# Kernel tuning notes

Hardware: AMD Instinct MI355X
Metric: run time of the kernel (lower is better)

## Reference

```python
import jax, jax.numpy as jnp
import numpy as np

NUM_GRAPHS = 256
N_NODES = 128          # nodes per graph (equal-size graphs)
DEG = 16               # average degree
NUM_EDGES = NUM_GRAPHS * N_NODES * DEG
NUM_HEADS = 8
SCALE = 10.0
INF_REPLACE = 1.0


def setup_inputs() -> dict:
    key = jax.random.key(0)
    k1, k2, k3 = jax.random.split(key, 3)
    # each graph owns a contiguous block of N_NODES global node ids
    eg = jnp.repeat(jnp.arange(NUM_GRAPHS, dtype=jnp.int32), N_NODES * DEG)
    src_loc = jax.random.randint(k1, (NUM_EDGES,), 0, N_NODES, dtype=jnp.int32)
    dst_loc = jax.random.randint(k2, (NUM_EDGES,), 0, N_NODES, dtype=jnp.int32)
    edge_index = jnp.stack([eg * N_NODES + src_loc, eg * N_NODES + dst_loc])  # [2, E]
    edge_weight = jax.random.uniform(k3, (NUM_EDGES,), minval=0.1, maxval=1.0)
    batch = jnp.repeat(jnp.arange(NUM_GRAPHS, dtype=jnp.int32), N_NODES)  # [N_total]
    return {
        'edge_index': edge_index,
        'edge_weight': edge_weight,
        'batch': batch,
        'num_graphs': NUM_GRAPHS,
        'max_num_nodes': N_NODES,
    }


def _shortest_path_bias(edge_index, edge_weight, batch, num_graphs, max_num_nodes):
    G, n = num_graphs, max_num_nodes
    inf = jnp.inf
    # per-graph node offsets (graphs occupy contiguous node-id blocks)
    counts = jnp.bincount(batch, length=G)
    offsets = jnp.concatenate([jnp.zeros((1,), counts.dtype), jnp.cumsum(counts)[:-1]])
    src, dst = edge_index[0], edge_index[1]
    eg = batch[src]                              # graph id of each edge
    u = src - offsets[eg]                        # local node ids
    v = dst - offsets[eg]
    # self-loops are skipped in the original (masked to +inf -> no-op under min)
    w = jnp.where(src == dst, inf, edge_weight)

    # init dense distance: inf off-diagonal, 0 on diagonal, edge weights scattered
    dist = jnp.full((G, n, n), inf, dtype=edge_weight.dtype)
    diag = jnp.arange(n)
    dist = dist.at[:, diag, diag].set(0.0)
    dist = dist.at[eg, u, v].min(w)

    # batched Floyd-Warshall: d[i,j] = min(d[i,j], d[i,k] + d[k,j]) for all graphs
    def body(d, k):
        col = jax.lax.dynamic_slice_in_dim(d, k, 1, axis=2)  # [G, n, 1] = d[:, :, k]
        row = jax.lax.dynamic_slice_in_dim(d, k, 1, axis=1)  # [G, 1, n] = d[:, k, :]
        return jnp.minimum(d, col + row), None
    dist, _ = jax.lax.scan(body, dist, jnp.arange(n))

    # replace unreachable with 2 * max finite distance (per graph)
    finite = jnp.isfinite(dist)
    fmax = jnp.max(jnp.where(finite, dist, -inf), axis=(1, 2), keepdims=True)
    unreach = jnp.where(jnp.isfinite(fmax), 2.0 * fmax, INF_REPLACE)
    dist = jnp.where(finite, dist, unreach)

    # normalize per graph and scale
    max_val = jnp.maximum(jnp.max(dist, axis=(1, 2), keepdims=True), 1e-8)
    bias = -SCALE * (dist / max_val)
    bias = jnp.nan_to_num(bias, nan=0.0, posinf=-1e6, neginf=-1e6)

    # expand over heads and flatten to [B*H, n, n]
    bias = jnp.broadcast_to(bias[:, None], (G, NUM_HEADS, n, n))
    return bias.reshape(G * NUM_HEADS, n, n)


def reference(edge_index, edge_weight, batch, num_graphs, max_num_nodes):
    return _shortest_path_bias(edge_index, edge_weight, batch, num_graphs, max_num_nodes)
```

## Files before the change

### kernel.cpp

```cpp
#include <hip/hip_runtime.h>

#define NHEADS 8
#define NN     128
#define NCELL  (NN * NN)
#define NT     512
#define SCALE_F 10.0f

typedef float nfloat4 __attribute__((ext_vector_type(4)));

#define RP_O 0
#define RP_N 2048
#define CP_As 4096
#define CP_Bs 6208
#define DP   8320
#define RED  8640

template<int CBN>
__device__ __forceinline__ void extract_panels(const float (&dd)[4][8], float* lds,
                                               const int kbn, const int t,
                                               const int rgrp, const int cgrp,
                                               const int cpbase)
{
    if ((rgrp >> 2) == kbn) {
        const int q = rgrp & 3;
        #pragma unroll
        for (int rr = 0; rr < 4; ++rr) {
            const int iloc = 4 * q + rr;
            #pragma unroll
            for (int c = 0; c < 2; ++c) {
                *reinterpret_cast<float4*>(
                    &lds[RP_O + iloc * 128 + (cgrp << 2) + (c << 6)]) =
                    make_float4(dd[rr][c*4+0], dd[rr][c*4+1],
                                dd[rr][c*4+2], dd[rr][c*4+3]);
            }
        }
        const int p = cgrp - 4 * (kbn & 3);
        if ((unsigned)p < 4u) {
            #pragma unroll
            for (int rr = 0; rr < 4; ++rr) {
                *reinterpret_cast<float4*>(&lds[DP + (4*q+rr) * 20 + (p << 2)]) =
                    make_float4(dd[rr][CBN+0], dd[rr][CBN+1],
                                dd[rr][CBN+2], dd[rr][CBN+3]);
            }
        }
    }
    {
        const int q2 = cgrp - 4 * (kbn & 3);
        if ((unsigned)q2 < 4u) {
            #pragma unroll
            for (int e = 0; e < 4; ++e) {
                const int m = 4 * q2 + e;
                *reinterpret_cast<float4*>(&lds[cpbase + m * 132 + (rgrp << 2)]) =
                    make_float4(dd[0][CBN+e], dd[1][CBN+e],
                                dd[2][CBN+e], dd[3][CBN+e]);
            }
        }
    }
}

__device__ __forceinline__ void closure(float* lds, const int t, const int kb)
{
    if ((t >> 6) == kb) {
        asm volatile("s_waitcnt lgkmcnt(0)" ::: "memory");
        const int l  = t & 63;
        const int i  = l & 15;
        const int jq = l >> 4;
        float4 v = *reinterpret_cast<const float4*>(&lds[DP + i*20 + (jq << 2)]);
        float T0 = v.x, T1 = v.y, T2 = v.z, T3 = v.w;
        #pragma unroll
        for (int k = 0; k < 16; ++k) {
            const int ksrc = ((k >> 2) << 4) | i;
            float dik;
            switch (k & 3) {
                case 0: dik = __shfl(T0, ksrc); break;
                case 1: dik = __shfl(T1, ksrc); break;
                case 2: dik = __shfl(T2, ksrc); break;
                default: dik = __shfl(T3, ksrc); break;
            }
            const int rsrc = (jq << 4) | k;
            const float r0 = __shfl(T0, rsrc);
            const float r1 = __shfl(T1, rsrc);
            const float r2 = __shfl(T2, rsrc);
            const float r3 = __shfl(T3, rsrc);
            T0 = fminf(T0, dik + r0);
            T1 = fminf(T1, dik + r1);
            T2 = fminf(T2, dik + r2);
            T3 = fminf(T3, dik + r3);
        }
        *reinterpret_cast<float4*>(&lds[DP + i*20 + (jq << 2)]) =
            make_float4(T0, T1, T2, T3);
    }
}

__device__ __forceinline__ void bprime(float* lds, const int t)
{
    if (t < 256) {
        const float INF = __builtin_huge_valf();
        const int k2 = t >> 5;
        const int ch = t & 31;
        float4 R[16];
        #pragma unroll
        for (int m = 0; m < 16; ++m)
            R[m] = *reinterpret_cast<const float4*>(&lds[RP_O + m*128 + (ch<<2)]);
        float da[16], db[16];
        #pragma unroll
        for (int c4 = 0; c4 < 4; ++c4) {
            float4 va = *reinterpret_cast<const float4*>(&lds[DP + (2*k2  )*20 + (c4<<2)]);
            float4 vb = *reinterpret_cast<const float4*>(&lds[DP + (2*k2+1)*20 + (c4<<2)]);
            da[c4*4+0]=va.x; da[c4*4+1]=va.y; da[c4*4+2]=va.z; da[c4*4+3]=va.w;
            db[c4*4+0]=vb.x; db[c4*4+1]=vb.y; db[c4*4+2]=vb.z; db[c4*4+3]=vb.w;
        }
        float aA[4] = {INF, INF, INF, INF};
        float aB[4] = {INF, INF, INF, INF};
        #pragma unroll
        for (int mp = 0; mp < 8; ++mp) {
            const int m0 = 2*mp, m1 = 2*mp + 1;
            const float rv0[4] = {R[m0].x, R[m0].y, R[m0].z, R[m0].w};
            const float rv1[4] = {R[m1].x, R[m1].y, R[m1].z, R[m1].w};
            #pragma unroll
            for (int e = 0; e < 4; ++e) {
                aA[e] = fminf(fminf(aA[e], da[m0] + rv0[e]), da[m1] + rv1[e]);
                aB[e] = fminf(fminf(aB[e], db[m0] + rv0[e]), db[m1] + rv1[e]);
            }
        }
        *reinterpret_cast<float4*>(&lds[RP_N + (2*k2  )*128 + (ch<<2)]) =
            make_float4(aA[0], aA[1], aA[2], aA[3]);
        *reinterpret_cast<float4*>(&lds[RP_N + (2*k2+1)*128 + (ch<<2)]) =
            make_float4(aB[0], aB[1], aB[2], aB[3]);
    }
}

__device__ __forceinline__ void cphase(float (&dd)[4][8], float* lds,
                                       const int rgrp, const int cgrp,
                                       const int cpbase)
{
    #pragma unroll
    for (int mq = 0; mq < 4; ++mq) {
        float4 cp[4], ra[4], rb[4];
        #pragma unroll
        for (int e = 0; e < 4; ++e) {
            const int m = 4*mq + e;
            cp[e] = *reinterpret_cast<const float4*>(&lds[cpbase + m*132 + (rgrp<<2)]);
            ra[e] = *reinterpret_cast<const float4*>(&lds[RP_N + m*128 + (cgrp<<2)]);
            rb[e] = *reinterpret_cast<const float4*>(&lds[RP_N + m*128 + (cgrp<<2) + 64]);
        }
        #pragma unroll
        for (int e2 = 0; e2 < 2; ++e2) {
            const float c0[4]  = {cp[2*e2].x, cp[2*e2].y, cp[2*e2].z, cp[2*e2].w};
            const float c1[4]  = {cp[2*e2+1].x, cp[2*e2+1].y, cp[2*e2+1].z, cp[2*e2+1].w};
            const float ra0[4] = {ra[2*e2].x, ra[2*e2].y, ra[2*e2].z, ra[2*e2].w};
            const float ra1[4] = {ra[2*e2+1].x, ra[2*e2+1].y, ra[2*e2+1].z, ra[2*e2+1].w};
            const float rb0[4] = {rb[2*e2].x, rb[2*e2].y, rb[2*e2].z, rb[2*e2].w};
            const float rb1[4] = {rb[2*e2+1].x, rb[2*e2+1].y, rb[2*e2+1].z, rb[2*e2+1].w};
            #pragma unroll
            for (int rr = 0; rr < 4; ++rr) {
                #pragma unroll
                for (int e = 0; e < 4; ++e) {
                    dd[rr][e]   = fminf(fminf(dd[rr][e],   c0[rr] + ra0[e]), c1[rr] + ra1[e]);
                    dd[rr][4+e] = fminf(fminf(dd[rr][4+e], c0[rr] + rb0[e]), c1[rr] + rb1[e]);
                }
            }
        }
    }
}

__global__ __launch_bounds__(NT, 2)
void spb_fw_kernel(const int* __restrict__ edge_index,
                   const float* __restrict__ edge_weight,
                   const int num_edges, const int epg,
                   float* __restrict__ out)
{
    __shared__ float lds[NCELL];
    const float INF = __builtin_huge_valf();
    const int t    = threadIdx.x;
    const int g    = blockIdx.x;
    const int cgrp = t & 15;
    const int rgrp = t >> 4;

    const int ebase = g * epg;
    int esrc[4], edst[4]; float ew[4];
    #pragma unroll
    for (int k = 0; k < 4; ++k) {
        int e = t + k * NT;
        e = (e < epg) ? e : (epg - 1);
        const int idx = ebase + e;
        esrc[k] = edge_index[idx];
        edst[k] = edge_index[num_edges + idx];
        ew[k]   = edge_weight[idx];
    }

    #pragma unroll
    for (int c = 0; c < 8; ++c) {
        const int m   = t + (c << 9);
        const int i   = m >> 5;
        const int scm = m & 31;
        const int c0  = (scm ^ (i & 7)) << 2;
        float4 v;
        v.x = (c0 + 0 == i) ? 0.0f : INF;
        v.y = (c0 + 1 == i) ? 0.0f : INF;
        v.z = (c0 + 2 == i) ? 0.0f : INF;
        v.w = (c0 + 3 == i) ? 0.0f : INF;
        *reinterpret_cast<float4*>(&lds[m << 2]) = v;
    }
    __syncthreads();

    #pragma unroll
    for (int k = 0; k < 4; ++k) {
        const int u = esrc[k] - g * NN;
        const int v = edst[k] - g * NN;
        if (u != v && (unsigned)u < (unsigned)NN && (unsigned)v < (unsigned)NN) {
            const int a = (u << 7) + (v ^ ((u & 7) << 2));
            atomicMin(reinterpret_cast<int*>(&lds[a]), __float_as_int(ew[k]));
        }
    }
    __syncthreads();

    float dd[4][8];
    #pragma unroll
    for (int rr = 0; rr < 4; ++rr) {
        const int i = (rgrp << 2) + rr;
        const int s = i & 7;
        #pragma unroll
        for (int c = 0; c < 2; ++c) {
            float4 v = *reinterpret_cast<const float4*>(
                &lds[(i << 7) + (((cgrp + 16*c) ^ s) << 2)]);
            dd[rr][c*4+0]=v.x; dd[rr][c*4+1]=v.y; dd[rr][c*4+2]=v.z; dd[rr][c*4+3]=v.w;
        }
    }
    __syncthreads();

    extract_panels<0>(dd, lds, 0, t, rgrp, cgrp, CP_As);
    #pragma unroll 1
    for (int kb = 0; kb < 8; ++kb) {
        closure(lds, t, kb);
        __syncthreads();
        bprime(lds, t);
        __syncthreads();
        cphase(dd, lds, rgrp, cgrp, (kb & 1) ? CP_Bs : CP_As);
        if (kb < 7) {
            const int kbn = kb + 1;
            const int cpb = (kbn & 1) ? CP_Bs : CP_As;
            if (kbn < 4) extract_panels<0>(dd, lds, kbn, t, rgrp, cgrp, cpb);
            else         extract_panels<4>(dd, lds, kbn, t, rgrp, cgrp, cpb);
        }
    }
    __syncthreads();

    float mF = 0.0f, mA = 0.0f;
    #pragma unroll
    for (int rr = 0; rr < 4; ++rr)
        #pragma unroll
        for (int j = 0; j < 8; ++j) {
            const float v = dd[rr][j];
            mA = fmaxf(mA, v);
            mF = fmaxf(mF, v < INF ? v : 0.0f);
        }
    #pragma unroll
    for (int o = 32; o > 0; o >>= 1) {
        mF = fmaxf(mF, __shfl_xor(mF, o));
        mA = fmaxf(mA, __shfl_xor(mA, o));
    }
    if ((t & 63) == 0) {
        lds[RED + ((t >> 6) << 1)]     = mF;
        lds[RED + ((t >> 6) << 1) + 1] = mA;
    }
    __syncthreads();
    mF = lds[RED]; mA = lds[RED + 1];
    #pragma unroll
    for (int wv = 1; wv < 8; ++wv) {
        mF = fmaxf(mF, lds[RED + wv*2]);
        mA = fmaxf(mA, lds[RED + wv*2 + 1]);
    }
    const float twoF  = 2.0f * mF;
    const float maxv  = fmaxf((mA == INF) ? twoF : mF, 1e-8f);
    const float nscal = -SCALE_F / maxv;

    float* const outg = out + (size_t)g * (NHEADS * NCELL);
    #pragma unroll
    for (int rr = 0; rr < 4; ++rr) {
        const int i = (rgrp << 2) + rr;
        #pragma unroll
        for (int c = 0; c < 2; ++c) {
            nfloat4 v;
            v.x = ((dd[rr][c*4+0] == INF) ? twoF : dd[rr][c*4+0]) * nscal;
            v.y = ((dd[rr][c*4+1] == INF) ? twoF : dd[rr][c*4+1]) * nscal;
            v.z = ((dd[rr][c*4+2] == INF) ? twoF : dd[rr][c*4+2]) * nscal;
            v.w = ((dd[rr][c*4+3] == INF) ? twoF : dd[rr][c*4+3]) * nscal;
            const int o = (i << 7) + (cgrp << 2) + (c << 6);
            #pragma unroll
            for (int h = 0; h < NHEADS; ++h) {
                __builtin_nontemporal_store(
                    v, reinterpret_cast<nfloat4*>(&outg[h * NCELL + o]));
            }
        }
    }
}

extern "C" void kernel_launch(void* const* d_in, const int* in_sizes, int n_in,
                              void* d_out, int out_size, void* d_ws, size_t ws_size,
                              hipStream_t stream)
{
    const int*   edge_index  = (const int*)d_in[0];
    const float* edge_w      = (const float*)d_in[1];
    const int E    = in_sizes[1];
    const int Ntot = in_sizes[2];
    const int G    = Ntot / NN;
    const int epg  = E / G;
    float* out = (float*)d_out;
    spb_fw_kernel<<<G, NT, 0, stream>>>(edge_index, edge_w, E, epg, out);
}
```

Measured before the change: 61.65 us.

## Double threads per block and fuse closure with B-panel update

Doubles the block to 1024 threads so each thread holds a 4x4 tile of the distance matrix instead of 4x8, which halves the per-thread C-phase work and register footprint. The diagonal closure and the row-panel (bprime) update are merged into one function run by the first four waves, with each wave redoing the closure redundantly, so one barrier per block step is removed. A barrier is added after panel extraction instead. The risk is that the 1024-thread block and the extra redundant closure work could limit occupancy or add idle waves during the serial phases.

```diff
diff --git a/kernel.cpp b/kernel.cpp
--- a/kernel.cpp
+++ b/kernel.cpp
@@ -3,7 +3,7 @@
 #define NHEADS 8
 #define NN     128
 #define NCELL  (NN * NN)
-#define NT     512
+#define NT     1024
 #define SCALE_F 10.0f
 
 typedef float nfloat4 __attribute__((ext_vector_type(4)));
@@ -12,60 +12,48 @@
 #define RP_N 2048
 #define CP_As 4096
 #define CP_Bs 6208
-#define DP   8320
+#define DPS  8320
 #define RED  8640
 
-template<int CBN>
-__device__ __forceinline__ void extract_panels(const float (&dd)[4][8], float* lds,
-                                               const int kbn, const int t,
-                                               const int rgrp, const int cgrp,
-                                               const int cpbase)
+__device__ __forceinline__ void extract_panels(const float (&dd)[4][4], float* lds,
+                                               const int kbn, const int rgrp,
+                                               const int cgrp, const int cpbase)
 {
     if ((rgrp >> 2) == kbn) {
-        const int q = rgrp & 3;
+        const int qb = (rgrp & 3) << 2;
         #pragma unroll
         for (int rr = 0; rr < 4; ++rr) {
-            const int iloc = 4 * q + rr;
-            #pragma unroll
-            for (int c = 0; c < 2; ++c) {
-                *reinterpret_cast<float4*>(
-                    &lds[RP_O + iloc * 128 + (cgrp << 2) + (c << 6)]) =
-                    make_float4(dd[rr][c*4+0], dd[rr][c*4+1],
-                                dd[rr][c*4+2], dd[rr][c*4+3]);
-            }
-        }
-        const int p = cgrp - 4 * (kbn & 3);
-        if ((unsigned)p < 4u) {
+            *reinterpret_cast<float4*>(&lds[RP_O + (qb+rr)*128 + (cgrp<<2)]) =
+                make_float4(dd[rr][0], dd[rr][1], dd[rr][2], dd[rr][3]);
+        }
+        if ((cgrp >> 2) == kbn) {
+            const int p = (cgrp & 3) << 2;
             #pragma unroll
             for (int rr = 0; rr < 4; ++rr) {
-                *reinterpret_cast<float4*>(&lds[DP + (4*q+rr) * 20 + (p << 2)]) =
-                    make_float4(dd[rr][CBN+0], dd[rr][CBN+1],
-                                dd[rr][CBN+2], dd[rr][CBN+3]);
-            }
-        }
-    }
-    {
-        const int q2 = cgrp - 4 * (kbn & 3);
-        if ((unsigned)q2 < 4u) {
-            #pragma unroll
-            for (int e = 0; e < 4; ++e) {
-                const int m = 4 * q2 + e;
-                *reinterpret_cast<float4*>(&lds[cpbase + m * 132 + (rgrp << 2)]) =
-                    make_float4(dd[0][CBN+e], dd[1][CBN+e],
-                                dd[2][CBN+e], dd[3][CBN+e]);
-            }
-        }
-    }
-}
-
-__device__ __forceinline__ void closure(float* lds, const int t, const int kb)
-{
-    if ((t >> 6) == kb) {
-        asm volatile("s_waitcnt lgkmcnt(0)" ::: "memory");
+                *reinterpret_cast<float4*>(&lds[DPS + (qb+rr)*20 + p]) =
+                    make_float4(dd[rr][0], dd[rr][1], dd[rr][2], dd[rr][3]);
+            }
+        }
+    }
+    if ((cgrp >> 2) == kbn) {
+        const int mb = (cgrp & 3) << 2;
+        #pragma unroll
+        for (int e = 0; e < 4; ++e) {
+            *reinterpret_cast<float4*>(&lds[cpbase + (mb+e)*132 + (rgrp<<2)]) =
+                make_float4(dd[0][e], dd[1][e], dd[2][e], dd[3][e]);
+        }
+    }
+}
+
+__device__ __forceinline__ void closure_bprime(float* lds, const int t)
+{
+    if (t < 256) {
+        const float INF = __builtin_huge_valf();
         const int l  = t & 63;
         const int i  = l & 15;
         const int jq = l >> 4;
-        float4 v = *reinterpret_cast<const float4*>(&lds[DP + i*20 + (jq << 2)]);
+        const int w  = t >> 6;
+        float4 v = *reinterpret_cast<const float4*>(&lds[DPS + i*20 + (jq<<2)]);
         float T0 = v.x, T1 = v.y, T2 = v.z, T3 = v.w;
         #pragma unroll
         for (int k = 0; k < 16; ++k) {
@@ -87,84 +75,75 @@
             T2 = fminf(T2, dik + r2);
             T3 = fminf(T3, dik + r3);
         }
-        *reinterpret_cast<float4*>(&lds[DP + i*20 + (jq << 2)]) =
+        *reinterpret_cast<float4*>(&lds[DPS + i*20 + (jq<<2)]) =
             make_float4(T0, T1, T2, T3);
-    }
-}
-
-__device__ __forceinline__ void bprime(float* lds, const int t)
-{
-    if (t < 256) {
-        const float INF = __builtin_huge_valf();
-        const int k2 = t >> 5;
-        const int ch = t & 31;
-        float4 R[16];
-        #pragma unroll
-        for (int m = 0; m < 16; ++m)
-            R[m] = *reinterpret_cast<const float4*>(&lds[RP_O + m*128 + (ch<<2)]);
-        float da[16], db[16];
-        #pragma unroll
-        for (int c4 = 0; c4 < 4; ++c4) {
-            float4 va = *reinterpret_cast<const float4*>(&lds[DP + (2*k2  )*20 + (c4<<2)]);
-            float4 vb = *reinterpret_cast<const float4*>(&lds[DP + (2*k2+1)*20 + (c4<<2)]);
-            da[c4*4+0]=va.x; da[c4*4+1]=va.y; da[c4*4+2]=va.z; da[c4*4+3]=va.w;
-            db[c4*4+0]=vb.x; db[c4*4+1]=vb.y; db[c4*4+2]=vb.z; db[c4*4+3]=vb.w;
-        }
-        float aA[4] = {INF, INF, INF, INF};
-        float aB[4] = {INF, INF, INF, INF};
+        asm volatile("s_waitcnt lgkmcnt(0)" ::: "memory");
+        const int r  = (w << 2) | jq;
+        const int j0 = i << 3;
+        float da[16];
+        #pragma unroll
+        for (int q = 0; q < 4; ++q) {
+            float4 d4 = *reinterpret_cast<const float4*>(&lds[DPS + r*20 + (q<<2)]);
+            da[4*q+0]=d4.x; da[4*q+1]=d4.y; da[4*q+2]=d4.z; da[4*q+3]=d4.w;
+        }
+        float aA[8];
+        #pragma unroll
+        for (int e = 0; e < 8; ++e) aA[e] = INF;
         #pragma unroll
         for (int mp = 0; mp < 8; ++mp) {
             const int m0 = 2*mp, m1 = 2*mp + 1;
-            const float rv0[4] = {R[m0].x, R[m0].y, R[m0].z, R[m0].w};
-            const float rv1[4] = {R[m1].x, R[m1].y, R[m1].z, R[m1].w};
+            float4 ra0 = *reinterpret_cast<const float4*>(&lds[RP_O + m0*128 + j0]);
+            float4 ra1 = *reinterpret_cast<const float4*>(&lds[RP_O + m0*128 + j0 + 4]);
+            float4 rb0 = *reinterpret_cast<const float4*>(&lds[RP_O + m1*128 + j0]);
+            float4 rb1 = *reinterpret_cast<const float4*>(&lds[RP_O + m1*128 + j0 + 4]);
+            const float a0[4] = {ra0.x, ra0.y, ra0.z, ra0.w};
+            const float a1[4] = {ra1.x, ra1.y, ra1.z, ra1.w};
+            const float b0[4] = {rb0.x, rb0.y, rb0.z, rb0.w};
+            const float b1[4] = {rb1.x, rb1.y, rb1.z, rb1.w};
             #pragma unroll
             for (int e = 0; e < 4; ++e) {
-                aA[e] = fminf(fminf(aA[e], da[m0] + rv0[e]), da[m1] + rv1[e]);
-                aB[e] = fminf(fminf(aB[e], db[m0] + rv0[e]), db[m1] + rv1[e]);
-            }
-        }
-        *reinterpret_cast<float4*>(&lds[RP_N + (2*k2  )*128 + (ch<<2)]) =
+                aA[e]   = fminf(fminf(aA[e],   da[m0] + a0[e]), da[m1] + b0[e]);
+                aA[4+e] = fminf(fminf(aA[4+e], da[m0] + a1[e]), da[m1] + b1[e]);
+            }
+        }
+        *reinterpret_cast<float4*>(&lds[RP_N + r*128 + j0]) =
             make_float4(aA[0], aA[1], aA[2], aA[3]);
-        *reinterpret_cast<float4*>(&lds[RP_N + (2*k2+1)*128 + (ch<<2)]) =
-            make_float4(aB[0], aB[1], aB[2], aB[3]);
-    }
-}
-
-__device__ __forceinline__ void cphase(float (&dd)[4][8], float* lds,
+        *reinterpret_cast<float4*>(&lds[RP_N + r*128 + j0 + 4]) =
+            make_float4(aA[4], aA[5], aA[6], aA[7]);
+    }
+}
+
+__device__ __forceinline__ void cphase(float (&dd)[4][4], float* lds,
                                        const int rgrp, const int cgrp,
                                        const int cpbase)
 {
     #pragma unroll
     for (int mq = 0; mq < 4; ++mq) {
-        float4 cp[4], ra[4], rb[4];
+        float4 cp[4], ra[4];
         #pragma unroll
         for (int e = 0; e < 4; ++e) {
             const int m = 4*mq + e;
             cp[e] = *reinterpret_cast<const float4*>(&lds[cpbase + m*132 + (rgrp<<2)]);
             ra[e] = *reinterpret_cast<const float4*>(&lds[RP_N + m*128 + (cgrp<<2)]);
-            rb[e] = *reinterpret_cast<const float4*>(&lds[RP_N + m*128 + (cgrp<<2) + 64]);
-        }
-        #pragma unroll
-        for (int e2 = 0; e2 < 2; ++e2) {
-            const float c0[4]  = {cp[2*e2].x, cp[2*e2].y, cp[2*e2].z, cp[2*e2].w};
-            const float c1[4]  = {cp[2*e2+1].x, cp[2*e2+1].y, cp[2*e2+1].z, cp[2*e2+1].w};
-            const float ra0[4] = {ra[2*e2].x, ra[2*e2].y, ra[2*e2].z, ra[2*e2].w};
-            const float ra1[4] = {ra[2*e2+1].x, ra[2*e2+1].y, ra[2*e2+1].z, ra[2*e2+1].w};
-            const float rb0[4] = {rb[2*e2].x, rb[2*e2].y, rb[2*e2].z, rb[2*e2].w};
-            const float rb1[4] = {rb[2*e2+1].x, rb[2*e2+1].y, rb[2*e2+1].z, rb[2*e2+1].w};
+        }
+        #pragma unroll
+        for (int ee = 0; ee < 2; ++ee) {
+            const float c0[4] = {cp[2*ee].x, cp[2*ee].y, cp[2*ee].z, cp[2*ee].w};
+            const float c1[4] = {cp[2*ee+1].x, cp[2*ee+1].y, cp[2*ee+1].z, cp[2*ee+1].w};
+            const float r0[4] = {ra[2*ee].x, ra[2*ee].y, ra[2*ee].z, ra[2*ee].w};
+            const float r1[4] = {ra[2*ee+1].x, ra[2*ee+1].y, ra[2*ee+1].z, ra[2*ee+1].w};
             #pragma unroll
             for (int rr = 0; rr < 4; ++rr) {
                 #pragma unroll
                 for (int e = 0; e < 4; ++e) {
-                    dd[rr][e]   = fminf(fminf(dd[rr][e],   c0[rr] + ra0[e]), c1[rr] + ra1[e]);
-                    dd[rr][4+e] = fminf(fminf(dd[rr][4+e], c0[rr] + rb0[e]), c1[rr] + rb1[e]);
+                    dd[rr][e] = fminf(fminf(dd[rr][e], c0[rr] + r0[e]), c1[rr] + r1[e]);
                 }
             }
         }
     }
 }
 
-__global__ __launch_bounds__(NT, 2)
+__global__ __launch_bounds__(NT, 4)
 void spb_fw_kernel(const int* __restrict__ edge_index,
                    const float* __restrict__ edge_weight,
                    const int num_edges, const int epg,
@@ -174,24 +153,23 @@
     const float INF = __builtin_huge_valf();
     const int t    = threadIdx.x;
     const int g    = blockIdx.x;
-    const int cgrp = t & 15;
-    const int rgrp = t >> 4;
+    const int cgrp = t & 31;
+    const int rgrp = t >> 5;
 
     const int ebase = g * epg;
-    int esrc[4], edst[4]; float ew[4];
-    #pragma unroll
-    for (int k = 0; k < 4; ++k) {
-        int e = t + k * NT;
+    int es[2], ed[2]; float ewt[2];
+    #pragma unroll
+    for (int k = 0; k < 2; ++k) {
+        int e = t + (k << 10);
         e = (e < epg) ? e : (epg - 1);
-        const int idx = ebase + e;
-        esrc[k] = edge_index[idx];
-        edst[k] = edge_index[num_edges + idx];
-        ew[k]   = edge_weight[idx];
-    }
-
-    #pragma unroll
-    for (int c = 0; c < 8; ++c) {
-        const int m   = t + (c << 9);
+        es[k]  = edge_index[ebase + e];
+        ed[k]  = edge_index[num_edges + ebase + e];
+        ewt[k] = edge_weight[ebase + e];
+    }
+
+    #pragma unroll
+    for (int c = 0; c < 4; ++c) {
+        const int m   = t + (c << 10);
         const int i   = m >> 5;
         const int scm = m & 31;
         const int c0  = (scm ^ (i & 7)) << 2;
@@ -205,52 +183,43 @@
     __syncthreads();
 
     #pragma unroll
-    for (int k = 0; k < 4; ++k) {
-        const int u = esrc[k] - g * NN;
-        const int v = edst[k] - g * NN;
+    for (int k = 0; k < 2; ++k) {
+        const int u = es[k] - g * NN;
+        const int v = ed[k] - g * NN;
         if (u != v && (unsigned)u < (unsigned)NN && (unsigned)v < (unsigned)NN) {
             const int a = (u << 7) + (v ^ ((u & 7) << 2));
-            atomicMin(reinterpret_cast<int*>(&lds[a]), __float_as_int(ew[k]));
-        }
-    }
-    __syncthreads();
-
-    float dd[4][8];
+            atomicMin(reinterpret_cast<int*>(&lds[a]), __float_as_int(ewt[k]));
+        }
+    }
+    __syncthreads();
+
+    float dd[4][4];
     #pragma unroll
     for (int rr = 0; rr < 4; ++rr) {
         const int i = (rgrp << 2) + rr;
-        const int s = i & 7;
-        #pragma unroll
-        for (int c = 0; c < 2; ++c) {
-            float4 v = *reinterpret_cast<const float4*>(
-                &lds[(i << 7) + (((cgrp + 16*c) ^ s) << 2)]);
-            dd[rr][c*4+0]=v.x; dd[rr][c*4+1]=v.y; dd[rr][c*4+2]=v.z; dd[rr][c*4+3]=v.w;
-        }
-    }
-    __syncthreads();
-
-    extract_panels<0>(dd, lds, 0, t, rgrp, cgrp, CP_As);
+        float4 v = *reinterpret_cast<const float4*>(
+            &lds[(i << 7) + ((cgrp ^ (i & 7)) << 2)]);
+        dd[rr][0]=v.x; dd[rr][1]=v.y; dd[rr][2]=v.z; dd[rr][3]=v.w;
+    }
+    __syncthreads();
+
+    extract_panels(dd, lds, 0, rgrp, cgrp, CP_As);
+    __syncthreads();
     #pragma unroll 1
     for (int kb = 0; kb < 8; ++kb) {
-        closure(lds, t, kb);
-        __syncthreads();
-        bprime(lds, t);
+        closure_bprime(lds, t);
         __syncthreads();
         cphase(dd, lds, rgrp, cgrp, (kb & 1) ? CP_Bs : CP_As);
-        if (kb < 7) {
-            const int kbn = kb + 1;
-            const int cpb = (kbn & 1) ? CP_Bs : CP_As;
-            if (kbn < 4) extract_panels<0>(dd, lds, kbn, t, rgrp, cgrp, cpb);
-            else         extract_panels<4>(dd, lds, kbn, t, rgrp, cgrp, cpb);
-        }
-    }
-    __syncthreads();
+        if (kb < 7)
+            extract_panels(dd, lds, kb + 1, rgrp, cgrp, ((kb+1) & 1) ? CP_Bs : CP_As);
+        __syncthreads();
+    }
 
     float mF = 0.0f, mA = 0.0f;
     #pragma unroll
     for (int rr = 0; rr < 4; ++rr)
         #pragma unroll
-        for (int j = 0; j < 8; ++j) {
+        for (int j = 0; j < 4; ++j) {
             const float v = dd[rr][j];
             mA = fmaxf(mA, v);
             mF = fmaxf(mF, v < INF ? v : 0.0f);
@@ -267,7 +236,7 @@
     __syncthreads();
     mF = lds[RED]; mA = lds[RED + 1];
     #pragma unroll
-    for (int wv = 1; wv < 8; ++wv) {
+    for (int wv = 1; wv < 16; ++wv) {
         mF = fmaxf(mF, lds[RED + wv*2]);
         mA = fmaxf(mA, lds[RED + wv*2 + 1]);
     }
@@ -279,19 +248,16 @@
     #pragma unroll
     for (int rr = 0; rr < 4; ++rr) {
         const int i = (rgrp << 2) + rr;
-        #pragma unroll
-        for (int c = 0; c < 2; ++c) {
-            nfloat4 v;
-            v.x = ((dd[rr][c*4+0] == INF) ? twoF : dd[rr][c*4+0]) * nscal;
-            v.y = ((dd[rr][c*4+1] == INF) ? twoF : dd[rr][c*4+1]) * nscal;
-            v.z = ((dd[rr][c*4+2] == INF) ? twoF : dd[rr][c*4+2]) * nscal;
-            v.w = ((dd[rr][c*4+3] == INF) ? twoF : dd[rr][c*4+3]) * nscal;
-            const int o = (i << 7) + (cgrp << 2) + (c << 6);
-            #pragma unroll
-            for (int h = 0; h < NHEADS; ++h) {
-                __builtin_nontemporal_store(
-                    v, reinterpret_cast<nfloat4*>(&outg[h * NCELL + o]));
-            }
+        nfloat4 v;
+        v.x = ((dd[rr][0] == INF) ? twoF : dd[rr][0]) * nscal;
+        v.y = ((dd[rr][1] == INF) ? twoF : dd[rr][1]) * nscal;
+        v.z = ((dd[rr][2] == INF) ? twoF : dd[rr][2]) * nscal;
+        v.w = ((dd[rr][3] == INF) ? twoF : dd[rr][3]) * nscal;
+        const int o = (i << 7) + (cgrp << 2);
+        #pragma unroll
+        for (int h = 0; h < NHEADS; ++h) {
+            __builtin_nontemporal_store(
+                v, reinterpret_cast<nfloat4*>(&outg[h * NCELL + o]));
         }
     }
 }
```

After: 67.46 us. 1.09x slower.

## Run blocked Floyd-Warshall in packed fp16 with contiguous 8-column thread tiles

Applied to the files above, without the earlier changes.

Stores the per-thread distance tile and the row and column panels as packed half-precision vectors and does the min-plus updates with packed fp16 add/min. Each thread now owns 8 contiguous columns instead of two split groups of 4, and LDS panel layouts are resized to match. The aim is to halve LDS traffic and double ALU throughput in the b-prime and c-phase updates. Distances lose precision with fp16 rounding and range, which may break tolerance against the fp32 reference.

```diff
diff --git a/kernel.cpp b/kernel.cpp
--- a/kernel.cpp
+++ b/kernel.cpp
@@ -6,54 +6,47 @@
 #define NT     512
 #define SCALE_F 10.0f
 
-typedef float nfloat4 __attribute__((ext_vector_type(4)));
-
-#define RP_O 0
-#define RP_N 2048
-#define CP_As 4096
-#define CP_Bs 6208
-#define DP   8320
-#define RED  8640
-
-template<int CBN>
-__device__ __forceinline__ void extract_panels(const float (&dd)[4][8], float* lds,
-                                               const int kbn, const int t,
+typedef float    nfloat4 __attribute__((ext_vector_type(4)));
+typedef _Float16 h4      __attribute__((ext_vector_type(4)));
+typedef _Float16 h8      __attribute__((ext_vector_type(8)));
+
+#define RPAD   136
+#define RP_O_H 0
+#define RP_N_H 2176
+#define CP_A_H 4352
+#define CP_B_H 6464
+#define DPS_F  4400
+#define RED_F  4720
+
+__device__ __forceinline__ void extract_panels(const h8 (&dd)[4], float* lds,
+                                               _Float16* ldsH, const int kbn,
                                                const int rgrp, const int cgrp,
-                                               const int cpbase)
+                                               const int cpH)
 {
     if ((rgrp >> 2) == kbn) {
-        const int q = rgrp & 3;
-        #pragma unroll
-        for (int rr = 0; rr < 4; ++rr) {
-            const int iloc = 4 * q + rr;
-            #pragma unroll
-            for (int c = 0; c < 2; ++c) {
-                *reinterpret_cast<float4*>(
-                    &lds[RP_O + iloc * 128 + (cgrp << 2) + (c << 6)]) =
-                    make_float4(dd[rr][c*4+0], dd[rr][c*4+1],
-                                dd[rr][c*4+2], dd[rr][c*4+3]);
-            }
-        }
-        const int p = cgrp - 4 * (kbn & 3);
-        if ((unsigned)p < 4u) {
+        const int qb = (rgrp & 3) << 2;
+        #pragma unroll
+        for (int rr = 0; rr < 4; ++rr)
+            *reinterpret_cast<h8*>(ldsH + RP_O_H + (qb+rr)*RPAD + (cgrp << 3)) = dd[rr];
+        if ((cgrp >> 1) == kbn) {
+            const int p = (cgrp & 1) << 3;
             #pragma unroll
             for (int rr = 0; rr < 4; ++rr) {
-                *reinterpret_cast<float4*>(&lds[DP + (4*q+rr) * 20 + (p << 2)]) =
-                    make_float4(dd[rr][CBN+0], dd[rr][CBN+1],
-                                dd[rr][CBN+2], dd[rr][CBN+3]);
+                *reinterpret_cast<float4*>(&lds[DPS_F + (qb+rr)*20 + p]) =
+                    make_float4((float)dd[rr][0], (float)dd[rr][1],
+                                (float)dd[rr][2], (float)dd[rr][3]);
+                *reinterpret_cast<float4*>(&lds[DPS_F + (qb+rr)*20 + p + 4]) =
+                    make_float4((float)dd[rr][4], (float)dd[rr][5],
+                                (float)dd[rr][6], (float)dd[rr][7]);
             }
         }
     }
-    {
-        const int q2 = cgrp - 4 * (kbn & 3);
-        if ((unsigned)q2 < 4u) {
-            #pragma unroll
-            for (int e = 0; e < 4; ++e) {
-                const int m = 4 * q2 + e;
-                *reinterpret_cast<float4*>(&lds[cpbase + m * 132 + (rgrp << 2)]) =
-                    make_float4(dd[0][CBN+e], dd[1][CBN+e],
-                                dd[2][CBN+e], dd[3][CBN+e]);
-            }
+    if ((cgrp >> 1) == kbn) {
+        const int lcb = (cgrp & 1) << 3;
+        #pragma unroll
+        for (int e = 0; e < 8; ++e) {
+            h4 v = {dd[0][e], dd[1][e], dd[2][e], dd[3][e]};
+            *reinterpret_cast<h4*>(ldsH + cpH + (lcb+e)*132 + (rgrp << 2)) = v;
         }
     }
 }
@@ -65,7 +58,7 @@
         const int l  = t & 63;
         const int i  = l & 15;
         const int jq = l >> 4;
-        float4 v = *reinterpret_cast<const float4*>(&lds[DP + i*20 + (jq << 2)]);
+        float4 v = *reinterpret_cast<const float4*>(&lds[DPS_F + i*20 + (jq << 2)]);
         float T0 = v.x, T1 = v.y, T2 = v.z, T3 = v.w;
         #pragma unroll
         for (int k = 0; k < 16; ++k) {
@@ -87,80 +80,44 @@
             T2 = fminf(T2, dik + r2);
             T3 = fminf(T3, dik + r3);
         }
-        *reinterpret_cast<float4*>(&lds[DP + i*20 + (jq << 2)]) =
+        *reinterpret_cast<float4*>(&lds[DPS_F + i*20 + (jq << 2)]) =
             make_float4(T0, T1, T2, T3);
     }
 }
 
-__device__ __forceinline__ void bprime(float* lds, const int t)
+__device__ __forceinline__ void bprime(float* lds, _Float16* ldsH, const int t)
 {
     if (t < 256) {
-        const float INF = __builtin_huge_valf();
-        const int k2 = t >> 5;
-        const int ch = t & 31;
-        float4 R[16];
-        #pragma unroll
-        for (int m = 0; m < 16; ++m)
-            R[m] = *reinterpret_cast<const float4*>(&lds[RP_O + m*128 + (ch<<2)]);
-        float da[16], db[16];
-        #pragma unroll
-        for (int c4 = 0; c4 < 4; ++c4) {
-            float4 va = *reinterpret_cast<const float4*>(&lds[DP + (2*k2  )*20 + (c4<<2)]);
-            float4 vb = *reinterpret_cast<const float4*>(&lds[DP + (2*k2+1)*20 + (c4<<2)]);
-            da[c4*4+0]=va.x; da[c4*4+1]=va.y; da[c4*4+2]=va.z; da[c4*4+3]=va.w;
-            db[c4*4+0]=vb.x; db[c4*4+1]=vb.y; db[c4*4+2]=vb.z; db[c4*4+3]=vb.w;
-        }
-        float aA[4] = {INF, INF, INF, INF};
-        float aB[4] = {INF, INF, INF, INF};
-        #pragma unroll
-        for (int mp = 0; mp < 8; ++mp) {
-            const int m0 = 2*mp, m1 = 2*mp + 1;
-            const float rv0[4] = {R[m0].x, R[m0].y, R[m0].z, R[m0].w};
-            const float rv1[4] = {R[m1].x, R[m1].y, R[m1].z, R[m1].w};
-            #pragma unroll
-            for (int e = 0; e < 4; ++e) {
-                aA[e] = fminf(fminf(aA[e], da[m0] + rv0[e]), da[m1] + rv1[e]);
-                aB[e] = fminf(fminf(aB[e], db[m0] + rv0[e]), db[m1] + rv1[e]);
-            }
-        }
-        *reinterpret_cast<float4*>(&lds[RP_N + (2*k2  )*128 + (ch<<2)]) =
-            make_float4(aA[0], aA[1], aA[2], aA[3]);
-        *reinterpret_cast<float4*>(&lds[RP_N + (2*k2+1)*128 + (ch<<2)]) =
-            make_float4(aB[0], aB[1], aB[2], aB[3]);
-    }
-}
-
-__device__ __forceinline__ void cphase(float (&dd)[4][8], float* lds,
-                                       const int rgrp, const int cgrp,
-                                       const int cpbase)
-{
-    #pragma unroll
-    for (int mq = 0; mq < 4; ++mq) {
-        float4 cp[4], ra[4], rb[4];
-        #pragma unroll
-        for (int e = 0; e < 4; ++e) {
-            const int m = 4*mq + e;
-            cp[e] = *reinterpret_cast<const float4*>(&lds[cpbase + m*132 + (rgrp<<2)]);
-            ra[e] = *reinterpret_cast<const float4*>(&lds[RP_N + m*128 + (cgrp<<2)]);
-            rb[e] = *reinterpret_cast<const float4*>(&lds[RP_N + m*128 + (cgrp<<2) + 64]);
-        }
-        #pragma unroll
-        for (int e2 = 0; e2 < 2; ++e2) {
-            const float c0[4]  = {cp[2*e2].x, cp[2*e2].y, cp[2*e2].z, cp[2*e2].w};
-            const float c1[4]  = {cp[2*e2+1].x, cp[2*e2+1].y, cp[2*e2+1].z, cp[2*e2+1].w};
-            const float ra0[4] = {ra[2*e2].x, ra[2*e2].y, ra[2*e2].z, ra[2*e2].w};
-            const float ra1[4] = {ra[2*e2+1].x, ra[2*e2+1].y, ra[2*e2+1].z, ra[2*e2+1].w};
-            const float rb0[4] = {rb[2*e2].x, rb[2*e2].y, rb[2*e2].z, rb[2*e2].w};
-            const float rb1[4] = {rb[2*e2+1].x, rb[2*e2+1].y, rb[2*e2+1].z, rb[2*e2+1].w};
-            #pragma unroll
-            for (int rr = 0; rr < 4; ++rr) {
-                #pragma unroll
-                for (int e = 0; e < 4; ++e) {
-                    dd[rr][e]   = fminf(fminf(dd[rr][e],   c0[rr] + ra0[e]), c1[rr] + ra1[e]);
-                    dd[rr][4+e] = fminf(fminf(dd[rr][4+e], c0[rr] + rb0[e]), c1[rr] + rb1[e]);
-                }
-            }
-        }
+        const int r  = t >> 4;
+        const int j8 = t & 15;
+        float da[16];
+        #pragma unroll
+        for (int q = 0; q < 4; ++q) {
+            float4 d4 = *reinterpret_cast<const float4*>(&lds[DPS_F + r*20 + (q << 2)]);
+            da[4*q+0]=d4.x; da[4*q+1]=d4.y; da[4*q+2]=d4.z; da[4*q+3]=d4.w;
+        }
+        h8 acc = (h8)(_Float16)__builtin_huge_valf();
+        #pragma unroll
+        for (int m = 0; m < 16; ++m) {
+            h8 rv = *reinterpret_cast<const h8*>(ldsH + RP_O_H + m*RPAD + (j8 << 3));
+            h8 d2 = (h8)(_Float16)da[m];
+            acc = __builtin_elementwise_min(acc, d2 + rv);
+        }
+        *reinterpret_cast<h8*>(ldsH + RP_N_H + r*RPAD + (j8 << 3)) = acc;
+    }
+}
+
+__device__ __forceinline__ void cphase(h8 (&dd)[4], _Float16* ldsH,
+                                       const int rgrp, const int cgrp, const int cpH)
+{
+    #pragma unroll
+    for (int m = 0; m < 16; ++m) {
+        h4 c4 = *reinterpret_cast<const h4*>(ldsH + cpH + m*132 + (rgrp << 2));
+        h8 r8 = *reinterpret_cast<const h8*>(ldsH + RP_N_H + m*RPAD + (cgrp << 3));
+        dd[0] = __builtin_elementwise_min(dd[0], (h8)(c4[0]) + r8);
+        dd[1] = __builtin_elementwise_min(dd[1], (h8)(c4[1]) + r8);
+        dd[2] = __builtin_elementwise_min(dd[2], (h8)(c4[2]) + r8);
+        dd[3] = __builtin_elementwise_min(dd[3], (h8)(c4[3]) + r8);
     }
 }
 
@@ -171,6 +128,7 @@
                    float* __restrict__ out)
 {
     __shared__ float lds[NCELL];
+    _Float16* const ldsH = reinterpret_cast<_Float16*>(lds);
     const float INF = __builtin_huge_valf();
     const int t    = threadIdx.x;
     const int g    = blockIdx.x;
@@ -215,34 +173,32 @@
     }
     __syncthreads();
 
-    float dd[4][8];
+    h8 dd[4];
     #pragma unroll
     for (int rr = 0; rr < 4; ++rr) {
         const int i = (rgrp << 2) + rr;
         const int s = i & 7;
-        #pragma unroll
-        for (int c = 0; c < 2; ++c) {
-            float4 v = *reinterpret_cast<const float4*>(
-                &lds[(i << 7) + (((cgrp + 16*c) ^ s) << 2)]);
-            dd[rr][c*4+0]=v.x; dd[rr][c*4+1]=v.y; dd[rr][c*4+2]=v.z; dd[rr][c*4+3]=v.w;
-        }
-    }
-    __syncthreads();
-
-    extract_panels<0>(dd, lds, 0, t, rgrp, cgrp, CP_As);
+        const int q0 = cgrp << 1;
+        float4 a = *reinterpret_cast<const float4*>(&lds[(i << 7) + (((q0  ) ^ s) << 2)]);
+        float4 b = *reinterpret_cast<const float4*>(&lds[(i << 7) + (((q0+1) ^ s) << 2)]);
+        h8 v;
+        v[0]=(_Float16)a.x; v[1]=(_Float16)a.y; v[2]=(_Float16)a.z; v[3]=(_Float16)a.w;
+        v[4]=(_Float16)b.x; v[5]=(_Float16)b.y; v[6]=(_Float16)b.z; v[7]=(_Float16)b.w;
+        dd[rr] = v;
+    }
+    __syncthreads();
+
+    extract_panels(dd, lds, ldsH, 0, rgrp, cgrp, CP_A_H);
     #pragma unroll 1
     for (int kb = 0; kb < 8; ++kb) {
         closure(lds, t, kb);
         __syncthreads();
-        bprime(lds, t);
+        bprime(lds, ldsH, t);
         __syncthreads();
-        cphase(dd, lds, rgrp, cgrp, (kb & 1) ? CP_Bs : CP_As);
-        if (kb < 7) {
-            const int kbn = kb + 1;
-            const int cpb = (kbn & 1) ? CP_Bs : CP_As;
-            if (kbn < 4) extract_panels<0>(dd, lds, kbn, t, rgrp, cgrp, cpb);
-            else         extract_panels<4>(dd, lds, kbn, t, rgrp, cgrp, cpb);
-        }
+        cphase(dd, ldsH, rgrp, cgrp, (kb & 1) ? CP_B_H : CP_A_H);
+        if (kb < 7)
+            extract_panels(dd, lds, ldsH, kb + 1, rgrp, cgrp,
+                           ((kb + 1) & 1) ? CP_B_H : CP_A_H);
     }
     __syncthreads();
 
@@ -250,10 +206,10 @@
     #pragma unroll
     for (int rr = 0; rr < 4; ++rr)
         #pragma unroll
-        for (int j = 0; j < 8; ++j) {
-            const float v = dd[rr][j];
-            mA = fmaxf(mA, v);
-            mF = fmaxf(mF, v < INF ? v : 0.0f);
+        for (int e = 0; e < 8; ++e) {
+            const float f = (float)dd[rr][e];
+            mA = fmaxf(mA, f);
+            mF = fmaxf(mF, f < INF ? f : 0.0f);
         }
     #pragma unroll
     for (int o = 32; o > 0; o >>= 1) {
@@ -261,15 +217,15 @@
         mA = fmaxf(mA, __shfl_xor(mA, o));
     }
     if ((t & 63) == 0) {
-        lds[RED + ((t >> 6) << 1)]     = mF;
-        lds[RED + ((t >> 6) << 1) + 1] = mA;
-    }
-    __syncthreads();
-    mF = lds[RED]; mA = lds[RED + 1];
+        lds[RED_F + ((t >> 6) << 1)]     = mF;
+        lds[RED_F + ((t >> 6) << 1) + 1] = mA;
+    }
+    __syncthreads();
+    mF = lds[RED_F]; mA = lds[RED_F + 1];
     #pragma unroll
     for (int wv = 1; wv < 8; ++wv) {
-        mF = fmaxf(mF, lds[RED + wv*2]);
-        mA = fmaxf(mA, lds[RED + wv*2 + 1]);
+        mF = fmaxf(mF, lds[RED_F + wv*2]);
+        mA = fmaxf(mA, lds[RED_F + wv*2 + 1]);
     }
     const float twoF  = 2.0f * mF;
     const float maxv  = fmaxf((mA == INF) ? twoF : mF, 1e-8f);
@@ -279,19 +235,20 @@
     #pragma unroll
     for (int rr = 0; rr < 4; ++rr) {
         const int i = (rgrp << 2) + rr;
-        #pragma unroll
-        for (int c = 0; c < 2; ++c) {
-            nfloat4 v;
-            v.x = ((dd[rr][c*4+0] == INF) ? twoF : dd[rr][c*4+0]) * nscal;
-            v.y = ((dd[rr][c*4+1] == INF) ? twoF : dd[rr][c*4+1]) * nscal;
-            v.z = ((dd[rr][c*4+2] == INF) ? twoF : dd[rr][c*4+2]) * nscal;
-            v.w = ((dd[rr][c*4+3] == INF) ? twoF : dd[rr][c*4+3]) * nscal;
-            const int o = (i << 7) + (cgrp << 2) + (c << 6);
-            #pragma unroll
-            for (int h = 0; h < NHEADS; ++h) {
-                __builtin_nontemporal_store(
-                    v, reinterpret_cast<nfloat4*>(&outg[h * NCELL + o]));
-            }
+        float f[8];
+        #pragma unroll
+        for (int e = 0; e < 8; ++e) {
+            const float x = (float)dd[rr][e];
+            f[e] = ((x == INF) ? twoF : x) * nscal;
+        }
+        nfloat4 va, vb;
+        va.x=f[0]; va.y=f[1]; va.z=f[2]; va.w=f[3];
+        vb.x=f[4]; vb.y=f[5]; vb.z=f[6]; vb.w=f[7];
+        const int o = (i << 7) + (cgrp << 3);
+        #pragma unroll
+        for (int h = 0; h < NHEADS; ++h) {
+            __builtin_nontemporal_store(va, reinterpret_cast<nfloat4*>(&outg[h * NCELL + o]));
+            __builtin_nontemporal_store(vb, reinterpret_cast<nfloat4*>(&outg[h * NCELL + o + 4]));
         }
     }
 }
```

Result: slower. 99.96 us (+62.2%).

## Fuse diagonal closure into previous iteration and spread B-phase over all threads

Applied to the files above, without the earlier changes.

The diagonal-block closure for the next k-block now runs right after that block's panels are extracted, at the end of the previous iteration. This removes one block-wide barrier per iteration of the blocked Floyd-Warshall loop. The row-panel (bprime) update now uses all 512 threads, one row each, instead of 256 threads handling two rows each. This halves per-thread work and register footprint in that phase, at the cost of more redundant LDS reads of the pivot panel.

```diff
diff --git a/kernel.cpp b/kernel.cpp
--- a/kernel.cpp
+++ b/kernel.cpp
@@ -12,7 +12,7 @@
 #define RP_N 2048
 #define CP_As 4096
 #define CP_Bs 6208
-#define DP   8320
+#define DPS  8320
 #define RED  8640
 
 template<int CBN>
@@ -38,7 +38,7 @@
         if ((unsigned)p < 4u) {
             #pragma unroll
             for (int rr = 0; rr < 4; ++rr) {
-                *reinterpret_cast<float4*>(&lds[DP + (4*q+rr) * 20 + (p << 2)]) =
+                *reinterpret_cast<float4*>(&lds[DPS + (4*q+rr) * 20 + (p << 2)]) =
                     make_float4(dd[rr][CBN+0], dd[rr][CBN+1],
                                 dd[rr][CBN+2], dd[rr][CBN+3]);
             }
@@ -58,14 +58,14 @@
     }
 }
 
-__device__ __forceinline__ void closure(float* lds, const int t, const int kb)
-{
-    if ((t >> 6) == kb) {
+__device__ __forceinline__ void closure(float* lds, const int t, const int kbn)
+{
+    if ((t >> 6) == kbn) {
         asm volatile("s_waitcnt lgkmcnt(0)" ::: "memory");
         const int l  = t & 63;
         const int i  = l & 15;
         const int jq = l >> 4;
-        float4 v = *reinterpret_cast<const float4*>(&lds[DP + i*20 + (jq << 2)]);
+        float4 v = *reinterpret_cast<const float4*>(&lds[DPS + i*20 + (jq << 2)]);
         float T0 = v.x, T1 = v.y, T2 = v.z, T3 = v.w;
         #pragma unroll
         for (int k = 0; k < 16; ++k) {
@@ -87,47 +87,33 @@
             T2 = fminf(T2, dik + r2);
             T3 = fminf(T3, dik + r3);
         }
-        *reinterpret_cast<float4*>(&lds[DP + i*20 + (jq << 2)]) =
+        *reinterpret_cast<float4*>(&lds[DPS + i*20 + (jq << 2)]) =
             make_float4(T0, T1, T2, T3);
     }
 }
 
 __device__ __forceinline__ void bprime(float* lds, const int t)
 {
-    if (t < 256) {
-        const float INF = __builtin_huge_valf();
-        const int k2 = t >> 5;
-        const int ch = t & 31;
-        float4 R[16];
-        #pragma unroll
-        for (int m = 0; m < 16; ++m)
-            R[m] = *reinterpret_cast<const float4*>(&lds[RP_O + m*128 + (ch<<2)]);
-        float da[16], db[16];
-        #pragma unroll
-        for (int c4 = 0; c4 < 4; ++c4) {
-            float4 va = *reinterpret_cast<const float4*>(&lds[DP + (2*k2  )*20 + (c4<<2)]);
-            float4 vb = *reinterpret_cast<const float4*>(&lds[DP + (2*k2+1)*20 + (c4<<2)]);
-            da[c4*4+0]=va.x; da[c4*4+1]=va.y; da[c4*4+2]=va.z; da[c4*4+3]=va.w;
-            db[c4*4+0]=vb.x; db[c4*4+1]=vb.y; db[c4*4+2]=vb.z; db[c4*4+3]=vb.w;
-        }
-        float aA[4] = {INF, INF, INF, INF};
-        float aB[4] = {INF, INF, INF, INF};
-        #pragma unroll
-        for (int mp = 0; mp < 8; ++mp) {
-            const int m0 = 2*mp, m1 = 2*mp + 1;
-            const float rv0[4] = {R[m0].x, R[m0].y, R[m0].z, R[m0].w};
-            const float rv1[4] = {R[m1].x, R[m1].y, R[m1].z, R[m1].w};
-            #pragma unroll
-            for (int e = 0; e < 4; ++e) {
-                aA[e] = fminf(fminf(aA[e], da[m0] + rv0[e]), da[m1] + rv1[e]);
-                aB[e] = fminf(fminf(aB[e], db[m0] + rv0[e]), db[m1] + rv1[e]);
-            }
-        }
-        *reinterpret_cast<float4*>(&lds[RP_N + (2*k2  )*128 + (ch<<2)]) =
-            make_float4(aA[0], aA[1], aA[2], aA[3]);
-        *reinterpret_cast<float4*>(&lds[RP_N + (2*k2+1)*128 + (ch<<2)]) =
-            make_float4(aB[0], aB[1], aB[2], aB[3]);
-    }
+    const float INF = __builtin_huge_valf();
+    const int r  = t >> 5;
+    const int j4 = (t & 31) << 2;
+    float da[16];
+    #pragma unroll
+    for (int q = 0; q < 4; ++q) {
+        float4 d4 = *reinterpret_cast<const float4*>(&lds[DPS + r*20 + (q << 2)]);
+        da[4*q+0]=d4.x; da[4*q+1]=d4.y; da[4*q+2]=d4.z; da[4*q+3]=d4.w;
+    }
+    float a0 = INF, a1 = INF, a2 = INF, a3 = INF;
+    #pragma unroll
+    for (int m = 0; m < 16; ++m) {
+        float4 rv = *reinterpret_cast<const float4*>(&lds[RP_O + m*128 + j4]);
+        a0 = fminf(a0, da[m] + rv.x);
+        a1 = fminf(a1, da[m] + rv.y);
+        a2 = fminf(a2, da[m] + rv.z);
+        a3 = fminf(a3, da[m] + rv.w);
+    }
+    *reinterpret_cast<float4*>(&lds[RP_N + r*128 + j4]) =
+        make_float4(a0, a1, a2, a3);
 }
 
 __device__ __forceinline__ void cphase(float (&dd)[4][8], float* lds,
@@ -230,10 +216,11 @@
     __syncthreads();
 
     extract_panels<0>(dd, lds, 0, t, rgrp, cgrp, CP_As);
+    closure(lds, t, 0);
+    __syncthreads();
+
     #pragma unroll 1
     for (int kb = 0; kb < 8; ++kb) {
-        closure(lds, t, kb);
-        __syncthreads();
         bprime(lds, t);
         __syncthreads();
         cphase(dd, lds, rgrp, cgrp, (kb & 1) ? CP_Bs : CP_As);
@@ -242,9 +229,10 @@
             const int cpb = (kbn & 1) ? CP_Bs : CP_As;
             if (kbn < 4) extract_panels<0>(dd, lds, kbn, t, rgrp, cgrp, cpb);
             else         extract_panels<4>(dd, lds, kbn, t, rgrp, cgrp, cpb);
-        }
-    }
-    __syncthreads();
+            closure(lds, t, kbn);
+        }
+        __syncthreads();
+    }
 
     float mF = 0.0f, mA = 0.0f;
     #pragma unroll
```

New measurement: 61.34 us. No clear change (-0.5%).
